# Optimization experiments

Measured on AMD Instinct MI355X. Metric: run time of the kernel, lower is better.

Reference implementation:

```python
import jax, jax.numpy as jnp
import numpy as np

D = 1024

def setup_inputs() -> dict:
    key = jax.random.key(0)
    ks = jax.random.split(key, 9)
    B, S = 4, 2048
    s = 1.0 / np.sqrt(D)
    return {
        "query": jax.random.normal(ks[0], (B, S, D), jnp.float32),
        "key": jax.random.normal(ks[1], (B, S, D), jnp.float32),
        "value": jax.random.normal(ks[2], (B, S, D), jnp.float32),
        "Wq": jax.random.normal(ks[3], (D, D), jnp.float32) * s,
        "bq": jax.random.normal(ks[4], (D,), jnp.float32) * 0.01,
        "Wk": jax.random.normal(ks[5], (D, D), jnp.float32) * s,
        "bk": jax.random.normal(ks[6], (D,), jnp.float32) * 0.01,
        "Wv": jax.random.normal(ks[7], (D, D), jnp.float32) * s,
        "bv": jax.random.normal(ks[8], (D,), jnp.float32) * 0.01,
    }

def reference(query, key, value, Wq, bq, Wk, bk, Wv, bv):
    scale = 1.0 / (query.shape[-1] ** 0.5)
    q = jnp.einsum('bsd,ed->bse', query, Wq) + bq  # nn.Linear: x @ W.T + b
    k = jnp.einsum('bsd,ed->bse', key, Wk) + bk
    v = jnp.einsum('bsd,ed->bse', value, Wv) + bv
    scores = jnp.einsum('bqd,bkd->bqk', q, k) * scale  # [B, Sq, Skv]
    w = jax.nn.softmax(scores, axis=-1)
    return jnp.einsum('bqk,bkd->bqd', w, v)
```

## Files before the change

### kernel.cpp

```cpp
#include <hip/hip_runtime.h>

typedef __bf16 bf16x8 __attribute__((ext_vector_type(8)));
typedef float f32x4 __attribute__((ext_vector_type(4)));
typedef unsigned short u16x8 __attribute__((ext_vector_type(8)));

__device__ inline unsigned short f2bf(float f) {
  union { float f; unsigned u; } a; a.f = f;
  return (unsigned short)((a.u + 0x7fffu + ((a.u >> 16) & 1u)) >> 16);
}
__device__ inline float bf2f(unsigned short h) {
  union { unsigned u; float f; } a; a.u = ((unsigned)h) << 16;
  return a.f;
}

struct CvtArgs {
  const float* src[6];
  unsigned short* dst[6];
};

__global__ __launch_bounds__(256) void cvt6(CvtArgs a) {
  long long i = (long long)blockIdx.x * 256 + threadIdx.x;
  int idx; long long off;
  if (i < 6291456LL) { idx = (int)(i >> 21); off = i & ((1LL << 21) - 1); }
  else { long long j = i - 6291456LL; idx = 3 + (int)(j >> 18); off = j & ((1LL << 18) - 1); }
  float4 v = ((const float4*)a.src[idx])[off];
  ushort4 o;
  o.x = f2bf(v.x); o.y = f2bf(v.y); o.z = f2bf(v.z); o.w = f2bf(v.w);
  ((ushort4*)a.dst[idx])[off] = o;
}

#define EPI_PROJ 0
#define EPI_SCALE 1
#define EPI_OUT 2

struct GP {
  const unsigned short* A;
  const unsigned short* B;
  unsigned short* C;
  unsigned short* outQ; unsigned short* outK; unsigned short* outV;
  const float* biasQ; const float* biasK; const float* biasV;
  long long batchA, batchB, batchC;
  int lda, ldb, ldc, K;
  float scale;
};

#define G2L(gp, lp) __builtin_amdgcn_global_load_lds( \
    (const __attribute__((address_space(1))) void*)(gp), \
    (__attribute__((address_space(3))) void*)(lp), 16, 0, 0)

#define MFMA_(d, a, b) d = __builtin_amdgcn_mfma_f32_16x16x32_bf16(a, b, d, 0, 0, 0)
#define SB0() __builtin_amdgcn_sched_barrier(0)
#define LGKM(n) do { asm volatile("s_waitcnt lgkmcnt(" #n ")" ::: "memory"); SB0(); } while (0)
#define VMC(n) do { asm volatile("s_waitcnt vmcnt(" #n ")" ::: "memory"); SB0(); } while (0)

template<int BM, int BN, int WMW, int WNW, int EPI>
__global__ __launch_bounds__(512, 2) void gemm2(GP p) {
  constexpr int WAVES_N = BN / WNW;
  constexpr int AMF = WMW / 16;
  constexpr int BNF = WNW / 16;
  constexpr int AH = AMF / 2, BH = BNF / 2;
  constexpr int AF_N = AH * 2;
  constexpr int NBA = BM / 64, NBB = BN / 64;
  static_assert((BM / WMW) * WAVES_N == 8, "8 waves");
  static_assert(BNF == 4, "BF_N==4 assumed by lgkm immediates");

  extern __shared__ char smem[];
  char* smA = smem;
  char* smB = smem + 2 * BM * 128;

  const int tid = threadIdx.x;
  const int lane = tid & 63;
  const int wid = tid >> 6;
  const int wm = wid / WAVES_N, wn = wid % WAVES_N;

  const int gx = gridDim.x, gy = gridDim.y;
  const int nwg = gx * gy * (int)gridDim.z;
  int orig = blockIdx.x + gx * (blockIdx.y + gy * blockIdx.z);
  int qq = nwg >> 3, rr_ = nwg & 7;
  int xcd = orig & 7, sl = orig >> 3;
  int wg = (xcd < rr_ ? xcd * (qq + 1) : rr_ * (qq + 1) + (xcd - rr_) * qq) + sl;
  int bx = wg % gx;
  int t2 = wg / gx;
  int by = t2 % gy;
  int z  = t2 / gy;

  const int m0 = by * BM, n0 = bx * BN;

  const long long lda2 = (long long)p.lda * 2;
  const long long ldb2 = (long long)p.ldb * 2;
  const char* Abase = (const char*)(p.A + (long long)z * p.batchA) + (long long)m0 * lda2;
  const char* Bbase = (const char*)(p.B + (long long)z * p.batchB) + (long long)n0 * ldb2;

  const int trow = tid >> 3;
  const int cs = (((tid & 7) ^ (trow & 7)) << 4);
  const char* srcA = Abase + (long long)trow * lda2 + cs;
  const char* srcB = Bbase + (long long)trow * ldb2 + cs;

  const int NT = p.K >> 6;

  const int aRowB = ((wm * WMW + (lane & 15)) << 7);
  const int bRowB = ((wn * WNW + (lane & 15)) << 7);
  const int csw = (lane & 7) << 4;
  const int ck0 = (((lane >> 4) << 4)) ^ csw;
  const int ck1 = ((((lane >> 4) << 4)) | 64) ^ csw;

  f32x4 acc[AMF][BNF];
#pragma unroll
  for (int i = 0; i < AMF; ++i)
#pragma unroll
    for (int j = 0; j < BNF; ++j) acc[i][j] = (f32x4){0.f, 0.f, 0.f, 0.f};

  bf16x8 aLo[AH][2], aHi[AH][2], bLo[BH][2], bHi[BH][2];

  auto stage = [&](int t) {
    char* dA = smA + (t & 1) * (BM * 128) + (tid << 4);
    char* dB = smB + (t & 1) * (BN * 128) + (tid << 4);
    const char* sA = srcA + (long long)t * 128;
    const char* sB = srcB + (long long)t * 128;
#pragma unroll
    for (int c = 0; c < NBA; ++c) G2L(sA + (long long)c * (lda2 << 6), dA + c * 8192);
#pragma unroll
    for (int c = 0; c < NBB; ++c) G2L(sB + (long long)c * (ldb2 << 6), dB + c * 8192);
  };
  auto readAh = [&](int t, int half, bf16x8 (&dst)[AH][2]) {
    const char* ra = smA + (t & 1) * (BM * 128) + aRowB + half * (AH * 2048);
#pragma unroll
    for (int mi = 0; mi < AH; ++mi) {
      dst[mi][0] = *(const bf16x8*)(ra + mi * 2048 + ck0);
      dst[mi][1] = *(const bf16x8*)(ra + mi * 2048 + ck1);
    }
  };
  auto readBh = [&](int t, int half, bf16x8 (&dst)[BH][2]) {
    const char* rb = smB + (t & 1) * (BN * 128) + bRowB + half * (BH * 2048);
#pragma unroll
    for (int ni = 0; ni < BH; ++ni) {
      dst[ni][0] = *(const bf16x8*)(rb + ni * 2048 + ck0);
      dst[ni][1] = *(const bf16x8*)(rb + ni * 2048 + ck1);
    }
  };
  auto quad = [&](int qa, int qb, bf16x8 (&A)[AH][2], bf16x8 (&B)[BH][2]) {
    __builtin_amdgcn_s_setprio(1);
#pragma unroll
    for (int mi = 0; mi < AH; ++mi)
#pragma unroll
      for (int ni = 0; ni < BH; ++ni) {
        MFMA_(acc[qa * AH + mi][qb * BH + ni], A[mi][0], B[ni][0]);
        MFMA_(acc[qa * AH + mi][qb * BH + ni], A[mi][1], B[ni][1]);
      }
    __builtin_amdgcn_s_setprio(0);
  };

  stage(0); stage(1);
  if constexpr (NBA + NBB == 8) VMC(8); else VMC(6);
  __builtin_amdgcn_s_barrier();
  readAh(0, 0, aLo); readBh(0, 0, bLo);
  SB0();

  for (int t = 0; t < NT; ++t) {
    readAh(t, 1, aHi);
    SB0();
    if constexpr (AF_N == 8) LGKM(8); else LGKM(4);
    quad(0, 0, aLo, bLo);
    readBh(t, 1, bHi);
    SB0();
    LGKM(4);
    quad(1, 0, aHi, bLo);
    LGKM(0);
    quad(0, 1, aLo, bHi);
    quad(1, 1, aHi, bHi);
    VMC(0);
    __builtin_amdgcn_s_barrier();
    if (t + 2 < NT) stage(t + 2);
    if (t + 1 < NT) { readAh(t + 1, 0, aLo); readBh(t + 1, 0, bLo); }
    SB0();
  }

  const int c0 = lane & 15;
  const int r0 = (lane >> 4) << 2;
  if constexpr (EPI == EPI_SCALE) {
    unsigned short* Cz = p.C + (long long)z * p.batchC;
#pragma unroll
    for (int mi = 0; mi < AMF; ++mi) {
      const int grow = m0 + wm * WMW + (mi << 4) + r0;
#pragma unroll
      for (int ni = 0; ni < BNF; ++ni) {
        const int gcol = n0 + wn * WNW + (ni << 4) + c0;
#pragma unroll
        for (int rr = 0; rr < 4; ++rr)
          Cz[(long long)(grow + rr) * p.ldc + gcol] = f2bf(acc[mi][ni][rr] * p.scale);
      }
    }
  } else if constexpr (EPI == EPI_OUT) {
    float* Cz = (float*)p.C + (long long)z * p.batchC;
#pragma unroll
    for (int mi = 0; mi < AMF; ++mi) {
      const int grow = m0 + wm * WMW + (mi << 4) + r0;
#pragma unroll
      for (int ni = 0; ni < BNF; ++ni) {
        const int gcol = n0 + wn * WNW + (ni << 4) + c0;
#pragma unroll
        for (int rr = 0; rr < 4; ++rr)
          Cz[(long long)(grow + rr) * p.ldc + gcol] = acc[mi][ni][rr] * p.scale;
      }
    }
  } else {
    if (z < 2) {
      unsigned short* O = (z == 0) ? p.outQ : p.outK;
      const float* bias = (z == 0) ? p.biasQ : p.biasK;
#pragma unroll
      for (int mi = 0; mi < AMF; ++mi) {
        const int grow = m0 + wm * WMW + (mi << 4) + r0;
#pragma unroll
        for (int ni = 0; ni < BNF; ++ni) {
          const int gcol = n0 + wn * WNW + (ni << 4) + c0;
          const float bb = bias[gcol];
#pragma unroll
          for (int rr = 0; rr < 4; ++rr)
            O[(long long)(grow + rr) * 1024 + gcol] = f2bf(acc[mi][ni][rr] + bb);
        }
      }
    } else {
#pragma unroll
      for (int mi = 0; mi < AMF; ++mi) {
        const int grow = m0 + wm * WMW + (mi << 4) + r0;
        const int bb = grow >> 11, s = grow & 2047;
#pragma unroll
        for (int ni = 0; ni < BNF; ++ni) {
          const int d = n0 + wn * WNW + (ni << 4) + c0;
          const float ba = p.biasV[d];
          ushort4 pk;
          pk.x = f2bf(acc[mi][ni][0] + ba);
          pk.y = f2bf(acc[mi][ni][1] + ba);
          pk.z = f2bf(acc[mi][ni][2] + ba);
          pk.w = f2bf(acc[mi][ni][3] + ba);
          *(ushort4*)(p.outV + ((long long)bb << 21) + (long long)d * 2048 + s) = pk;
        }
      }
    }
  }
}

__global__ __launch_bounds__(256) void softmax_rows(unsigned short* __restrict__ S) {
  const size_t row = blockIdx.x;
  unsigned short* pp = S + row * 2048;
  const int t = threadIdx.x, lane = t & 63, wave = t >> 6;
  u16x8 h = ((const u16x8*)pp)[t];
  float x[8];
#pragma unroll
  for (int j = 0; j < 8; ++j) x[j] = bf2f(h[j]);
  float m = x[0];
#pragma unroll
  for (int j = 1; j < 8; ++j) m = fmaxf(m, x[j]);
#pragma unroll
  for (int off = 32; off >= 1; off >>= 1) m = fmaxf(m, __shfl_xor(m, off, 64));
  __shared__ float rmax[4], rsum[4];
  if (lane == 0) rmax[wave] = m;
  __syncthreads();
  m = fmaxf(fmaxf(rmax[0], rmax[1]), fmaxf(rmax[2], rmax[3]));
  float e[8], sum = 0.f;
#pragma unroll
  for (int j = 0; j < 8; ++j) { e[j] = __expf(x[j] - m); sum += e[j]; }
#pragma unroll
  for (int off = 32; off >= 1; off >>= 1) sum += __shfl_xor(sum, off, 64);
  if (lane == 0) rsum[wave] = sum;
  __syncthreads();
  sum = rsum[0] + rsum[1] + rsum[2] + rsum[3];
  const float inv = 1.f / sum;
  u16x8 o;
#pragma unroll
  for (int j = 0; j < 8; ++j) o[j] = f2bf(e[j] * inv);
  ((u16x8*)pp)[t] = o;
}

extern "C" void kernel_launch(void* const* d_in, const int* in_sizes, int n_in,
                              void* d_out, int out_size, void* d_ws, size_t ws_size,
                              hipStream_t stream) {
  const float* q  = (const float*)d_in[0];
  const float* k  = (const float*)d_in[1];
  const float* v  = (const float*)d_in[2];
  const float* Wq = (const float*)d_in[3];
  const float* bq = (const float*)d_in[4];
  const float* Wk = (const float*)d_in[5];
  const float* bk = (const float*)d_in[6];
  const float* Wv = (const float*)d_in[7];
  const float* bv = (const float*)d_in[8];

  unsigned short* Xb = (unsigned short*)d_ws;
  unsigned short* Wb = Xb + 25165824;
  unsigned short* qb = Wb + 3145728;
  unsigned short* kb = qb + 8388608;
  unsigned short* vT = kb + 8388608;
  unsigned short* S  = Xb;

  (void)hipFuncSetAttribute((const void*)gemm2<256,128,64,64,EPI_PROJ>,
      hipFuncAttributeMaxDynamicSharedMemorySize, 98304);
  (void)hipFuncSetAttribute((const void*)gemm2<256,256,128,64,EPI_SCALE>,
      hipFuncAttributeMaxDynamicSharedMemorySize, 131072);
  (void)hipFuncSetAttribute((const void*)gemm2<256,128,64,64,EPI_OUT>,
      hipFuncAttributeMaxDynamicSharedMemorySize, 98304);

  CvtArgs ca;
  ca.src[0] = q;  ca.src[1] = k;  ca.src[2] = v;
  ca.src[3] = Wq; ca.src[4] = Wk; ca.src[5] = Wv;
  ca.dst[0] = Xb;            ca.dst[1] = Xb + 8388608; ca.dst[2] = Xb + 16777216;
  ca.dst[3] = Wb;            ca.dst[4] = Wb + 1048576; ca.dst[5] = Wb + 2097152;
  cvt6<<<27648, 256, 0, stream>>>(ca);

  GP gp{};
  gp.A = Xb;  gp.batchA = 8388608; gp.lda = 1024;
  gp.B = Wb;  gp.batchB = 1048576; gp.ldb = 1024;
  gp.outQ = qb; gp.outK = kb; gp.outV = vT;
  gp.biasQ = bq; gp.biasK = bk; gp.biasV = bv;
  gp.K = 1024; gp.scale = 1.f;
  gemm2<256,128,64,64,EPI_PROJ><<<dim3(8, 32, 3), 512, 98304, stream>>>(gp);

  GP gs{};
  gs.A = qb; gs.batchA = 2097152; gs.lda = 1024;
  gs.B = kb; gs.batchB = 2097152; gs.ldb = 1024;
  gs.C = S;  gs.batchC = 4194304; gs.ldc = 2048;
  gs.K = 1024; gs.scale = 0.03125f;
  gemm2<256,256,128,64,EPI_SCALE><<<dim3(8, 8, 4), 512, 131072, stream>>>(gs);

  softmax_rows<<<8192, 256, 0, stream>>>(S);

  GP gv{};
  gv.A = S;  gv.batchA = 4194304; gv.lda = 2048;
  gv.B = vT; gv.batchB = 2097152; gv.ldb = 2048;
  gv.C = (unsigned short*)d_out; gv.batchC = 2097152; gv.ldc = 1024;
  gv.K = 2048; gv.scale = 1.f;
  gemm2<256,128,64,64,EPI_OUT><<<dim3(8, 8, 4), 512, 98304, stream>>>(gv);
}
```

Measured before the change: 178.7 us.

## Fuse fp32-to-bf16 activation conversion into projection GEMM A-tile loads

Removes the separate conversion pass over the three fp32 activation tensors. The projection GEMM now loads fp32 A tiles into registers, converts them to bf16 and writes them to LDS with a one-tile-ahead register prefetch, while B still uses direct global-to-LDS loads. Only the weights go through a small conversion kernel. The projection tile also grows to 256x256, and the workspace layout shrinks. This saves one write and one reread of the bf16 activations, but adds register pressure and synchronous LDS writes inside the main loop, and the larger tile gives fewer workgroups.

New measurement: 281.2 us. 57.3% more time.

```diff
diff --git a/kernel.cpp b/kernel.cpp
--- a/kernel.cpp
+++ b/kernel.cpp
@@ -13,20 +13,18 @@
   return a.f;
 }
 
-struct CvtArgs {
-  const float* src[6];
-  unsigned short* dst[6];
-};
-
-__global__ __launch_bounds__(256) void cvt6(CvtArgs a) {
-  long long i = (long long)blockIdx.x * 256 + threadIdx.x;
-  int idx; long long off;
-  if (i < 6291456LL) { idx = (int)(i >> 21); off = i & ((1LL << 21) - 1); }
-  else { long long j = i - 6291456LL; idx = 3 + (int)(j >> 18); off = j & ((1LL << 18) - 1); }
-  float4 v = ((const float4*)a.src[idx])[off];
+__global__ __launch_bounds__(256) void cvtW(const float* __restrict__ Wq,
+                                            const float* __restrict__ Wk,
+                                            const float* __restrict__ Wv,
+                                            unsigned short* __restrict__ Wb) {
+  int i = blockIdx.x * 256 + threadIdx.x;
+  int idx = i >> 18;
+  int off = i & 262143;
+  const float* s = (idx == 0) ? Wq : ((idx == 1) ? Wk : Wv);
+  float4 v = ((const float4*)s)[off];
   ushort4 o;
   o.x = f2bf(v.x); o.y = f2bf(v.y); o.z = f2bf(v.z); o.w = f2bf(v.w);
-  ((ushort4*)a.dst[idx])[off] = o;
+  ((ushort4*)(Wb + idx * 1048576))[off] = o;
 }
 
 #define EPI_PROJ 0
@@ -39,6 +37,7 @@
   unsigned short* C;
   unsigned short* outQ; unsigned short* outK; unsigned short* outV;
   const float* biasQ; const float* biasK; const float* biasV;
+  const float* Af0; const float* Af1; const float* Af2;
   long long batchA, batchB, batchC;
   int lda, ldb, ldc, K;
   float scale;
@@ -53,16 +52,15 @@
 #define LGKM(n) do { asm volatile("s_waitcnt lgkmcnt(" #n ")" ::: "memory"); SB0(); } while (0)
 #define VMC(n) do { asm volatile("s_waitcnt vmcnt(" #n ")" ::: "memory"); SB0(); } while (0)
 
-template<int BM, int BN, int WMW, int WNW, int EPI>
+template<int BM, int BN, int WMW, int WNW, int EPI, bool ACVT>
 __global__ __launch_bounds__(512, 2) void gemm2(GP p) {
   constexpr int WAVES_N = BN / WNW;
   constexpr int AMF = WMW / 16;
   constexpr int BNF = WNW / 16;
   constexpr int AH = AMF / 2, BH = BNF / 2;
-  constexpr int AF_N = AH * 2;
   constexpr int NBA = BM / 64, NBB = BN / 64;
   static_assert((BM / WMW) * WAVES_N == 8, "8 waves");
-  static_assert(BNF == 4, "BF_N==4 assumed by lgkm immediates");
+  static_assert(BNF == 4, "lgkm immediates assume BNF==4");
 
   extern __shared__ char smem[];
   char* smA = smem;
@@ -86,15 +84,23 @@
 
   const int m0 = by * BM, n0 = bx * BN;
 
-  const long long lda2 = (long long)p.lda * 2;
   const long long ldb2 = (long long)p.ldb * 2;
-  const char* Abase = (const char*)(p.A + (long long)z * p.batchA) + (long long)m0 * lda2;
   const char* Bbase = (const char*)(p.B + (long long)z * p.batchB) + (long long)n0 * ldb2;
 
   const int trow = tid >> 3;
   const int cs = (((tid & 7) ^ (trow & 7)) << 4);
-  const char* srcA = Abase + (long long)trow * lda2 + cs;
   const char* srcB = Bbase + (long long)trow * ldb2 + cs;
+
+  const long long lda2 = (long long)p.lda * 2;
+  const char* srcA = nullptr;
+  const float* AzF = nullptr;
+  if constexpr (ACVT) {
+    const float* Az = (z == 0) ? p.Af0 : ((z == 1) ? p.Af1 : p.Af2);
+    AzF = Az + (long long)(m0 + trow) * p.lda + (tid & 7) * 8;
+  } else {
+    const char* Abase = (const char*)(p.A + (long long)z * p.batchA) + (long long)m0 * lda2;
+    srcA = Abase + (long long)trow * lda2 + cs;
+  }
 
   const int NT = p.K >> 6;
 
@@ -111,6 +117,7 @@
     for (int j = 0; j < BNF; ++j) acc[i][j] = (f32x4){0.f, 0.f, 0.f, 0.f};
 
   bf16x8 aLo[AH][2], aHi[AH][2], bLo[BH][2], bHi[BH][2];
+  float4 areg[ACVT ? 2 * NBA : 1];
 
   auto stage = [&](int t) {
     char* dA = smA + (t & 1) * (BM * 128) + (tid << 4);
@@ -122,6 +129,32 @@
 #pragma unroll
     for (int c = 0; c < NBB; ++c) G2L(sB + (long long)c * (ldb2 << 6), dB + c * 8192);
   };
+  auto stageB = [&](int t) {
+    char* dB = smB + (t & 1) * (BN * 128) + (tid << 4);
+    const char* sB = srcB + (long long)t * 128;
+#pragma unroll
+    for (int c = 0; c < NBB; ++c) G2L(sB + (long long)c * (ldb2 << 6), dB + c * 8192);
+  };
+  auto ldA = [&](int t) {
+    const float* s0 = AzF + (long long)t * 64;
+#pragma unroll
+    for (int c = 0; c < NBA; ++c) {
+      const float* s = s0 + (long long)c * 64 * p.lda;
+      areg[2 * c]     = *(const float4*)(s);
+      areg[2 * c + 1] = *(const float4*)(s + 4);
+    }
+  };
+  auto wrA = [&](int t) {
+    char* dA = smA + (t & 1) * (BM * 128) + (trow << 7) + cs;
+#pragma unroll
+    for (int c = 0; c < NBA; ++c) {
+      float4 lo = areg[2 * c], hi = areg[2 * c + 1];
+      union { bf16x8 v; uint4 q; } u;
+      u.v = (bf16x8){(__bf16)lo.x, (__bf16)lo.y, (__bf16)lo.z, (__bf16)lo.w,
+                     (__bf16)hi.x, (__bf16)hi.y, (__bf16)hi.z, (__bf16)hi.w};
+      *(uint4*)(dA + c * 8192) = u.q;
+    }
+  };
   auto readAh = [&](int t, int half, bf16x8 (&dst)[AH][2]) {
     const char* ra = smA + (t & 1) * (BM * 128) + aRowB + half * (AH * 2048);
 #pragma unroll
@@ -150,16 +183,23 @@
     __builtin_amdgcn_s_setprio(0);
   };
 
-  stage(0); stage(1);
-  if constexpr (NBA + NBB == 8) VMC(8); else VMC(6);
+  if constexpr (ACVT) {
+    ldA(0); stageB(0); stageB(1);
+    VMC(8);
+    wrA(0); LGKM(0);
+  } else {
+    stage(0); stage(1);
+    if constexpr (NBA + NBB == 8) VMC(8); else VMC(6);
+  }
   __builtin_amdgcn_s_barrier();
+  if constexpr (ACVT) ldA(1);
   readAh(0, 0, aLo); readBh(0, 0, bLo);
   SB0();
 
   for (int t = 0; t < NT; ++t) {
     readAh(t, 1, aHi);
     SB0();
-    if constexpr (AF_N == 8) LGKM(8); else LGKM(4);
+    if constexpr (AH * 2 == 8) LGKM(8); else LGKM(4);
     quad(0, 0, aLo, bLo);
     readBh(t, 1, bHi);
     SB0();
@@ -169,8 +209,12 @@
     quad(0, 1, aLo, bHi);
     quad(1, 1, aHi, bHi);
     VMC(0);
+    if constexpr (ACVT) { if (t + 1 < NT) wrA(t + 1); LGKM(0); }
     __builtin_amdgcn_s_barrier();
-    if (t + 2 < NT) stage(t + 2);
+    if (t + 2 < NT) {
+      if constexpr (ACVT) { ldA(t + 2); stageB(t + 2); }
+      else stage(t + 2);
+    }
     if (t + 1 < NT) { readAh(t + 1, 0, aLo); readBh(t + 1, 0, bLo); }
     SB0();
   }
@@ -285,41 +329,35 @@
   const float* Wv = (const float*)d_in[7];
   const float* bv = (const float*)d_in[8];
 
-  unsigned short* Xb = (unsigned short*)d_ws;
-  unsigned short* Wb = Xb + 25165824;
+  unsigned short* S  = (unsigned short*)d_ws;
+  unsigned short* Wb = S + 16777216;
   unsigned short* qb = Wb + 3145728;
   unsigned short* kb = qb + 8388608;
   unsigned short* vT = kb + 8388608;
-  unsigned short* S  = Xb;
-
-  (void)hipFuncSetAttribute((const void*)gemm2<256,128,64,64,EPI_PROJ>,
+
+  (void)hipFuncSetAttribute((const void*)gemm2<256,256,128,64,EPI_PROJ,true>,
+      hipFuncAttributeMaxDynamicSharedMemorySize, 131072);
+  (void)hipFuncSetAttribute((const void*)gemm2<256,256,128,64,EPI_SCALE,false>,
+      hipFuncAttributeMaxDynamicSharedMemorySize, 131072);
+  (void)hipFuncSetAttribute((const void*)gemm2<256,128,64,64,EPI_OUT,false>,
       hipFuncAttributeMaxDynamicSharedMemorySize, 98304);
-  (void)hipFuncSetAttribute((const void*)gemm2<256,256,128,64,EPI_SCALE>,
-      hipFuncAttributeMaxDynamicSharedMemorySize, 131072);
-  (void)hipFuncSetAttribute((const void*)gemm2<256,128,64,64,EPI_OUT>,
-      hipFuncAttributeMaxDynamicSharedMemorySize, 98304);
-
-  CvtArgs ca;
-  ca.src[0] = q;  ca.src[1] = k;  ca.src[2] = v;
-  ca.src[3] = Wq; ca.src[4] = Wk; ca.src[5] = Wv;
-  ca.dst[0] = Xb;            ca.dst[1] = Xb + 8388608; ca.dst[2] = Xb + 16777216;
-  ca.dst[3] = Wb;            ca.dst[4] = Wb + 1048576; ca.dst[5] = Wb + 2097152;
-  cvt6<<<27648, 256, 0, stream>>>(ca);
+
+  cvtW<<<3072, 256, 0, stream>>>(Wq, Wk, Wv, Wb);
 
   GP gp{};
-  gp.A = Xb;  gp.batchA = 8388608; gp.lda = 1024;
   gp.B = Wb;  gp.batchB = 1048576; gp.ldb = 1024;
+  gp.Af0 = q; gp.Af1 = k; gp.Af2 = v; gp.lda = 1024;
   gp.outQ = qb; gp.outK = kb; gp.outV = vT;
   gp.biasQ = bq; gp.biasK = bk; gp.biasV = bv;
   gp.K = 1024; gp.scale = 1.f;
-  gemm2<256,128,64,64,EPI_PROJ><<<dim3(8, 32, 3), 512, 98304, stream>>>(gp);
+  gemm2<256,256,128,64,EPI_PROJ,true><<<dim3(4, 32, 3), 512, 131072, stream>>>(gp);
 
   GP gs{};
   gs.A = qb; gs.batchA = 2097152; gs.lda = 1024;
   gs.B = kb; gs.batchB = 2097152; gs.ldb = 1024;
   gs.C = S;  gs.batchC = 4194304; gs.ldc = 2048;
   gs.K = 1024; gs.scale = 0.03125f;
-  gemm2<256,256,128,64,EPI_SCALE><<<dim3(8, 8, 4), 512, 131072, stream>>>(gs);
+  gemm2<256,256,128,64,EPI_SCALE,false><<<dim3(8, 8, 4), 512, 131072, stream>>>(gs);
 
   softmax_rows<<<8192, 256, 0, stream>>>(S);
 
@@ -328,5 +366,5 @@
   gv.B = vT; gv.batchB = 2097152; gv.ldb = 2048;
   gv.C = (unsigned short*)d_out; gv.batchC = 2097152; gv.ldc = 1024;
   gv.K = 2048; gv.scale = 1.f;
-  gemm2<256,128,64,64,EPI_OUT><<<dim3(8, 8, 4), 512, 98304, stream>>>(gv);
-}
+  gemm2<256,128,64,64,EPI_OUT,false><<<dim3(8, 8, 4), 512, 98304, stream>>>(gv);
+}
```
